# Performance work log

Measured on AMD Instinct MI355X. Metric: run time of the kernel, lower is better.

Reference implementation:

```python
import jax, jax.numpy as jnp
import numpy as np

B, T, D_MODEL = 4, 2048, 1024
D_EXPERT, N_EXPERTS, TOP_K = 4096, 8, 2
CAPACITY_FACTOR = 1.25
AUX_COEFF, Z_COEFF = 0.01, 0.001


def setup_inputs() -> dict:
    key = jax.random.key(0)
    k = jax.random.split(key, 4)
    x = jax.random.normal(k[0], (B, T, D_MODEL), jnp.float32)
    Wr = jax.random.normal(k[1], (D_MODEL, N_EXPERTS), jnp.float32) * 0.02
    W1 = jax.random.normal(k[2], (N_EXPERTS, D_MODEL, D_EXPERT), jnp.float32) * (1.0 / np.sqrt(D_MODEL))
    b1 = jnp.zeros((N_EXPERTS, D_EXPERT), jnp.float32)
    W2 = jax.random.normal(k[3], (N_EXPERTS, D_EXPERT, D_MODEL), jnp.float32) * (1.0 / np.sqrt(D_EXPERT))
    b2 = jnp.zeros((N_EXPERTS, D_MODEL), jnp.float32)
    return {"x": x, "Wr": Wr, "W1": W1, "b1": b1, "W2": W2, "b2": b2}


def reference(x, Wr, W1, b1, W2, b2):
    Bb, Tt, D = x.shape
    N = Bb * Tt
    E = W1.shape[0]
    capacity = max(1, int(N / E * CAPACITY_FACTOR * TOP_K))

    xf = x.reshape(N, D)
    logits = xf @ Wr                                    # (N, E)
    z_loss = jnp.mean(jax.nn.logsumexp(logits, axis=-1) ** 2)
    probs = jax.nn.softmax(logits, axis=-1)             # (N, E)

    topk_p, topk_i = jax.lax.top_k(probs, TOP_K)        # (N, K)
    # one-hot expert mask (top-k experts are distinct per token)
    mask = jnp.zeros((N, E), probs.dtype).at[jnp.arange(N)[:, None], topk_i].set(1.0)

    # capacity truncation: keep first `capacity` assigned tokens per expert, in token order
    pos = (jnp.cumsum(mask, axis=0) - mask).astype(jnp.int32)   # exclusive rank within expert
    keep = (pos < capacity) & (mask > 0)
    mask_t = jnp.where(keep, mask, jnp.zeros_like(mask))

    # Switch-style aux loss on truncated mask
    total_sel = jnp.maximum(mask_t.sum(), 1.0)
    f_i = mask_t.sum(axis=0) / total_sel
    P_i = probs.mean(axis=0)
    aux_loss = E * jnp.sum(f_i * P_i)

    # normalized top-k combine weights (differentiable through probs)
    tk_raw = jnp.take_along_axis(probs, topk_i, axis=1)          # (N, K)
    tk = tk_raw / jnp.maximum(tk_raw.sum(axis=-1, keepdims=True), 1e-9)

    # dispatch tokens into (E, capacity, D) buffer; dropped tokens scatter out of range
    pos_safe = jnp.where(keep, pos, capacity)                    # capacity -> dropped
    pos_k = jnp.take_along_axis(pos_safe, topk_i, axis=1)        # (N, K)
    upd = jnp.broadcast_to(xf[:, None, :], (N, TOP_K, D)).reshape(-1, D)
    buf = jnp.zeros((E, capacity, D), x.dtype).at[topk_i.reshape(-1), pos_k.reshape(-1)].set(upd, mode='drop')

    # grouped expert MLP
    h = jax.nn.relu(jnp.einsum('ecd,edf->ecf', buf, W1) + b1[:, None, :])
    eo = jnp.einsum('ecf,efd->ecd', h, W2) + b2[:, None, :]      # (E, capacity, D)

    # combine: gather each token's top-k expert outputs, weight, sum; dropped -> weight 0
    valid_k = jnp.take_along_axis(keep, topk_i, axis=1)          # (N, K) bool
    w = tk * valid_k.astype(tk.dtype)
    pos_g = jnp.minimum(pos_k, capacity - 1)
    gathered = eo[topk_i, pos_g]                                 # (N, K, D)
    out = jnp.einsum('nk,nkd->nd', w, gathered).reshape(Bb, Tt, D)

    total_aux = AUX_COEFF * aux_loss + Z_COEFF * z_loss
    return out, aux_loss, z_loss, total_aux
```

## Files before the change

kernel.cpp:

```cpp
#include <hip/hip_runtime.h>
#include <stdint.h>

#define N_TOK    8192
#define DM       1024
#define DE       4096
#define NEXP     8
#define CAP      2560
#define AUX_CO   0.01f
#define Z_CO     0.001f

typedef __attribute__((ext_vector_type(4))) float f32x4;
typedef __attribute__((ext_vector_type(8))) __bf16 bf16x8;

static __device__ __forceinline__ unsigned short f2bf(float f) {
  union { float f; uint32_t u; } v; v.f = f;
  uint32_t r = 0x7fffu + ((v.u >> 16) & 1u);
  return (unsigned short)((v.u + r) >> 16);
}
static __device__ __forceinline__ float bf2f(unsigned short u) {
  union { uint32_t u; float f; } v; v.u = ((uint32_t)u) << 16;
  return v.f;
}

#define MEMFENCE() asm volatile("" ::: "memory")
#define BAR()    do { MEMFENCE(); __builtin_amdgcn_s_barrier(); MEMFENCE(); } while (0)
#define LGKM0()  asm volatile("s_waitcnt lgkmcnt(0)" ::: "memory")
#define VMW(N)   asm volatile("s_waitcnt vmcnt(" #N ")" ::: "memory")
#define GLD16(g, l) __builtin_amdgcn_global_load_lds( \
    (const __attribute__((address_space(1))) void*)(g), \
    (__attribute__((address_space(3))) void*)(l), 16, 0, 0)

__global__ __launch_bounds__(256) void transpose_to_bf16(
    const float* __restrict__ in, unsigned short* __restrict__ out, int R, int C)
{
  __shared__ float tile[64][65];
  const size_t eoff = (size_t)blockIdx.z * R * C;
  const int bx = blockIdx.x * 64, by = blockIdx.y * 64;
  const int r = threadIdx.x >> 2, c16 = (threadIdx.x & 3) * 16;
#pragma unroll
  for (int j = 0; j < 4; ++j) {
    const float4 v = *(const float4*)&in[eoff + (size_t)(by + r) * C + bx + c16 + j * 4];
    tile[r][c16 + j * 4 + 0] = v.x; tile[r][c16 + j * 4 + 1] = v.y;
    tile[r][c16 + j * 4 + 2] = v.z; tile[r][c16 + j * 4 + 3] = v.w;
  }
  __syncthreads();
  const int oc = threadIdx.x >> 2, r16 = (threadIdx.x & 3) * 16;
#pragma unroll
  for (int half = 0; half < 2; ++half) {
    uint4 o;
    const int rb = r16 + half * 8;
    o.x = (uint32_t)f2bf(tile[rb + 0][oc]) | ((uint32_t)f2bf(tile[rb + 1][oc]) << 16);
    o.y = (uint32_t)f2bf(tile[rb + 2][oc]) | ((uint32_t)f2bf(tile[rb + 3][oc]) << 16);
    o.z = (uint32_t)f2bf(tile[rb + 4][oc]) | ((uint32_t)f2bf(tile[rb + 5][oc]) << 16);
    o.w = (uint32_t)f2bf(tile[rb + 6][oc]) | ((uint32_t)f2bf(tile[rb + 7][oc]) << 16);
    *(uint4*)&out[eoff + (size_t)(bx + oc) * R + by + rb] = o;
  }
}

__global__ __launch_bounds__(256) void router_kernel(
    const float* __restrict__ x, const float* __restrict__ Wr,
    int* __restrict__ topk, float* __restrict__ tkw, float* __restrict__ zP)
{
  const int tid = threadIdx.x, lane = tid & 63, wave = tid >> 6;
  float zacc = 0.f;
  float pacc[NEXP];
#pragma unroll
  for (int e = 0; e < NEXP; ++e) pacc[e] = 0.f;

  for (int it = 0; it < 4; ++it) {
    const int t = blockIdx.x * 16 + it * 4 + wave;
    float acc[NEXP];
#pragma unroll
    for (int e = 0; e < NEXP; ++e) acc[e] = 0.f;
    const f32x4* x4 = (const f32x4*)(x + (size_t)t * DM);
#pragma unroll
    for (int i = 0; i < 4; ++i) {
      f32x4 xv = x4[i * 64 + lane];
#pragma unroll
      for (int j = 0; j < 4; ++j) {
        const float xs = xv[j];
        const float* wr = Wr + (size_t)((i * 64 + lane) * 4 + j) * NEXP;
#pragma unroll
        for (int e = 0; e < NEXP; ++e) acc[e] += xs * wr[e];
      }
    }
#pragma unroll
    for (int m = 32; m; m >>= 1)
#pragma unroll
      for (int e = 0; e < NEXP; ++e) acc[e] += __shfl_xor(acc[e], m);

    float mx = acc[0];
#pragma unroll
    for (int e = 1; e < NEXP; ++e) mx = fmaxf(mx, acc[e]);
    float p[NEXP], s = 0.f;
#pragma unroll
    for (int e = 0; e < NEXP; ++e) { p[e] = expf(acc[e] - mx); s += p[e]; }
    const float lse = mx + logf(s);
    zacc += lse * lse;
    const float inv_s = 1.f / s;
#pragma unroll
    for (int e = 0; e < NEXP; ++e) pacc[e] += p[e] * inv_s;

    int e0 = 0; float v0 = p[0];
#pragma unroll
    for (int e = 1; e < NEXP; ++e) if (p[e] > v0) { v0 = p[e]; e0 = e; }
    int e1 = -1; float v1 = -1.f;
#pragma unroll
    for (int e = 0; e < NEXP; ++e) if (e != e0 && p[e] > v1) { v1 = p[e]; e1 = e; }

    const float pr0 = v0 * inv_s, pr1 = v1 * inv_s;
    const float denom = fmaxf(pr0 + pr1, 1e-9f);
    if (lane == 0) {
      topk[2*t]   = e0; topk[2*t+1] = e1;
      tkw[2*t]    = pr0 / denom; tkw[2*t+1] = pr1 / denom;
    }
  }
  __shared__ float blk[4][9];
  if (lane == 0) {
    blk[wave][0] = zacc;
#pragma unroll
    for (int e = 0; e < NEXP; ++e) blk[wave][1 + e] = pacc[e];
  }
  __syncthreads();
  if (tid < 9)
    zP[blockIdx.x * 9 + tid] = blk[0][tid] + blk[1][tid] + blk[2][tid] + blk[3][tid];
}

__global__ __launch_bounds__(512) void scan_kernel(
    const int2* __restrict__ topk, const float2* __restrict__ tkw,
    int* __restrict__ posk, float* __restrict__ wts,
    int* __restrict__ inv, int* __restrict__ kept)
{
  __shared__ int2   stopk[N_TOK];
  __shared__ float2 stkw[N_TOK];
  const int tid = threadIdx.x;
  for (int j = tid; j < N_TOK; j += 512) { stopk[j] = topk[j]; stkw[j] = tkw[j]; }
  __syncthreads();

  const int lane = tid & 63;
  const int e = tid >> 6;
  int base = 0;
  const uint64_t below = (lane == 63) ? 0xFFFFFFFFFFFFFFFFull >> 1
                                      : ((1ull << lane) - 1ull);
  for (int i = 0; i < N_TOK / 64; ++i) {
    const int t = i * 64 + lane;
    const int2 ti = stopk[t];
    const float2 w = stkw[t];
    const bool hit = (ti.x == e) || (ti.y == e);
    const uint64_t m = __ballot(hit);
    if (hit) {
      const int pos = base + (int)__popcll(m & below);
      const bool kp = pos < CAP;
      const int k = (ti.x == e) ? 0 : 1;
      posk[2*t + k] = kp ? pos : CAP;
      wts[2*t + k]  = kp ? ((k == 0) ? w.x : w.y) : 0.f;
      if (kp) inv[e * CAP + pos] = t;
    }
    base += (int)__popcll(m);
  }
  const int tail = base < CAP ? base : CAP;
  for (int q = tail + lane; q < CAP; q += 64) inv[e * CAP + q] = -1;
  if (lane == 0) kept[e] = tail;
}

__global__ __launch_bounds__(256) void dispatch_kernel(
    const float* __restrict__ x, const int* __restrict__ inv,
    unsigned short* __restrict__ buf)
{
  const int slot = blockIdx.x;
  const int t = inv[slot];
  ushort4 o;
  if (t >= 0) {
    const f32x4 v = ((const f32x4*)(x + (size_t)t * DM))[threadIdx.x];
    o.x = f2bf(v[0]); o.y = f2bf(v[1]); o.z = f2bf(v[2]); o.w = f2bf(v[3]);
  } else {
    o.x = 0; o.y = 0; o.z = 0; o.w = 0;
  }
  ((ushort4*)(buf + (size_t)slot * DM))[threadIdx.x] = o;
}

template<bool RELU, bool BIAS>
__global__ __launch_bounds__(512, 2) void gemm2b(
    const unsigned short* __restrict__ A,
    const unsigned short* __restrict__ Bt,
    const float* __restrict__ bias,
    unsigned short* __restrict__ C,
    const int* __restrict__ kept,
    int M, int N, int K, int lda, int mt, int nt, int nsplit, int nwg)
{
  __shared__ __attribute__((aligned(16))) unsigned short As[2 * 16384];
  __shared__ __attribute__((aligned(16))) unsigned short Bs[2 * 16384];
  const int tid = threadIdx.x, lane = tid & 63, wave = tid >> 6;
  const int wr = wave >> 2, wc = wave & 3;
  const int frow = lane & 15, kgrp = lane >> 4;

  int wg = (int)blockIdx.x;
  wg = (wg & 7) * (nwg >> 3) + (wg >> 3);
  const int ntpe = mt * nt;
  const int bpe = ntpe * nsplit;
  const int e = wg / bpe;
  const int rem = wg % bpe;
  const int split = rem / ntpe;
  const int rr = rem % ntpe;
  const int m0 = (rr / nt) * 256;
  const int n0 = (rr % nt) * 256;
  if (m0 >= kept[e]) return;

  const unsigned short* Ae = A  + (size_t)e * M * lda + (size_t)m0 * lda + (size_t)split * K;
  const unsigned short* Be = Bt + (size_t)e * N * lda + (size_t)n0 * lda + (size_t)split * K;

  const int srow = tid >> 3;
  const int scol = ((tid & 7) ^ (srow & 7)) * 8;

  auto stage = [&](int t) {
    const int c = t & 1, k0 = t * 64;
#pragma unroll
    for (int i = 0; i < 4; ++i)
      GLD16(Ae + (size_t)(i * 64 + srow) * lda + (k0 + scol),
            &As[c * 16384 + i * 4096 + tid * 8]);
#pragma unroll
    for (int i = 0; i < 4; ++i)
      GLD16(Be + (size_t)(i * 64 + srow) * lda + (k0 + scol),
            &Bs[c * 16384 + i * 4096 + tid * 8]);
  };
  auto rdA = [&](bf16x8* dst, int c, int mh) {
#pragma unroll
    for (int m = 0; m < 4; ++m) {
      const int row = wr * 128 + mh * 64 + m * 16 + frow;
#pragma unroll
      for (int kk = 0; kk < 2; ++kk)
        dst[m * 2 + kk] = *(const bf16x8*)
          &As[c * 16384 + row * 64 + (((kk * 4 + kgrp) ^ (row & 7)) * 8)];
    }
  };
  auto rdB = [&](bf16x8* dst, int c, int nh) {
#pragma unroll
    for (int n = 0; n < 2; ++n) {
      const int row = wc * 64 + nh * 32 + n * 16 + frow;
#pragma unroll
      for (int kk = 0; kk < 2; ++kk)
        dst[n * 2 + kk] = *(const bf16x8*)
          &Bs[c * 16384 + row * 64 + (((kk * 4 + kgrp) ^ (row & 7)) * 8)];
    }
  };

  f32x4 acc[8][4];
#pragma unroll
  for (int m = 0; m < 8; ++m)
#pragma unroll
    for (int n = 0; n < 4; ++n) acc[m][n] = (f32x4){0.f, 0.f, 0.f, 0.f};

  bf16x8 af0[8], af1[8], bq0[4], bq1[4];
  auto mfmaQ = [&](int mh, int nh, bf16x8* af, bf16x8* bq) {
#pragma unroll
    for (int m = 0; m < 4; ++m)
#pragma unroll
      for (int n = 0; n < 2; ++n)
#pragma unroll
        for (int kk = 0; kk < 2; ++kk)
          acc[mh * 4 + m][nh * 2 + n] = __builtin_amdgcn_mfma_f32_16x16x32_bf16(
              af[m * 2 + kk], bq[n * 2 + kk], acc[mh * 4 + m][nh * 2 + n], 0, 0, 0);
  };

  const int nk = K >> 6;

  stage(0); stage(1);

  for (int t = 0; t < nk; ++t) {
    const int c = t & 1;
    if (t + 2 <= nk) { VMW(8); } else { VMW(0); }
    BAR();
    rdA(af0, c, 0);
    rdA(af1, c, 1);
    rdB(bq0, c, 0);
    rdB(bq1, c, 1);
    LGKM0();
    BAR();
    if (t + 2 < nk) stage(t + 2);
    __builtin_amdgcn_s_setprio(1);
    mfmaQ(0, 0, af0, bq0);
    mfmaQ(0, 1, af0, bq1);
    mfmaQ(1, 0, af1, bq0);
    mfmaQ(1, 1, af1, bq1);
    __builtin_amdgcn_s_setprio(0);
  }

  unsigned short* Ce = C + (size_t)(split * NEXP + e) * M * N;
  const int r0 = m0 + wr * 128 + 4 * kgrp;
  const int c0 = n0 + wc * 64 + frow;
#pragma unroll
  for (int nf = 0; nf < 4; ++nf) {
    const int cc = c0 + nf * 16;
    float bv = 0.f;
    if (BIAS) bv = bias[(size_t)e * N + cc];
#pragma unroll
    for (int m = 0; m < 8; ++m) {
#pragma unroll
      for (int r = 0; r < 4; ++r) {
        float v = acc[m][nf][r] + bv;
        if (RELU) v = fmaxf(v, 0.f);
        Ce[(size_t)(r0 + m * 16 + r) * N + cc] = f2bf(v);
      }
    }
  }
}

__global__ __launch_bounds__(256) void combine_kernel(
    const unsigned short* __restrict__ eo2,
    const float* __restrict__ b2,
    const int* __restrict__ posk, const float* __restrict__ wts,
    const int* __restrict__ topk,
    const float* __restrict__ zP, const int* __restrict__ kept,
    float* __restrict__ out, float* __restrict__ outs)
{
  const int t = blockIdx.x;
  const int e0 = topk[2*t], e1 = topk[2*t+1];
  int p0 = posk[2*t], p1 = posk[2*t+1];
  p0 = p0 < CAP - 1 ? p0 : CAP - 1;
  p1 = p1 < CAP - 1 ? p1 : CAP - 1;
  const float w0 = wts[2*t], w1 = wts[2*t+1];
  const size_t o0 = ((size_t)e0 * CAP + p0) * DM;
  const size_t o1 = ((size_t)e1 * CAP + p1) * DM;
  const size_t sp = (size_t)NEXP * CAP * DM;
  const ushort4 a0 = ((const ushort4*)(eo2 + o0))[threadIdx.x];
  const ushort4 a1 = ((const ushort4*)(eo2 + sp + o0))[threadIdx.x];
  const ushort4 c0 = ((const ushort4*)(eo2 + o1))[threadIdx.x];
  const ushort4 c1 = ((const ushort4*)(eo2 + sp + o1))[threadIdx.x];
  const f32x4 bv0 = ((const f32x4*)(b2 + (size_t)e0 * DM))[threadIdx.x];
  const f32x4 bv1 = ((const f32x4*)(b2 + (size_t)e1 * DM))[threadIdx.x];
  f32x4 o;
  o[0] = w0 * (bf2f(a0.x) + bf2f(a1.x) + bv0[0]) + w1 * (bf2f(c0.x) + bf2f(c1.x) + bv1[0]);
  o[1] = w0 * (bf2f(a0.y) + bf2f(a1.y) + bv0[1]) + w1 * (bf2f(c0.y) + bf2f(c1.y) + bv1[1]);
  o[2] = w0 * (bf2f(a0.z) + bf2f(a1.z) + bv0[2]) + w1 * (bf2f(c0.z) + bf2f(c1.z) + bv1[2]);
  o[3] = w0 * (bf2f(a0.w) + bf2f(a1.w) + bv0[3]) + w1 * (bf2f(c0.w) + bf2f(c1.w) + bv1[3]);
  ((f32x4*)(out + (size_t)t * DM))[threadIdx.x] = o;

  if (t == 0 && threadIdx.x < 64) {
    const int lane = threadIdx.x;
    float v[9];
#pragma unroll
    for (int e = 0; e < 9; ++e) {
      float s = 0.f;
      for (int bk = 0; bk < 8; ++bk) s += zP[(lane * 8 + bk) * 9 + e];
      v[e] = s;
    }
#pragma unroll
    for (int m = 32; m; m >>= 1)
#pragma unroll
      for (int e = 0; e < 9; ++e) v[e] += __shfl_xor(v[e], m);
    if (lane == 0) {
      const float z = v[0] / (float)N_TOK;
      float total = 0.f;
      for (int e = 0; e < NEXP; ++e) total += (float)kept[e];
      total = fmaxf(total, 1.f);
      float aux = 0.f;
      for (int e = 0; e < NEXP; ++e)
        aux += ((float)kept[e] / total) * (v[1 + e] / (float)N_TOK);
      aux *= (float)NEXP;
      outs[0] = aux;
      outs[1] = z;
      outs[2] = AUX_CO * aux + Z_CO * z;
    }
  }
}

extern "C" void kernel_launch(void* const* d_in, const int* in_sizes, int n_in,
                              void* d_out, int out_size, void* d_ws, size_t ws_size,
                              hipStream_t stream)
{
  const float* x  = (const float*)d_in[0];
  const float* Wr = (const float*)d_in[1];
  const float* W1 = (const float*)d_in[2];
  const float* b1 = (const float*)d_in[3];
  const float* W2 = (const float*)d_in[4];
  const float* b2 = (const float*)d_in[5];
  float* out = (float*)d_out;

  char* p = (char*)d_ws;
  auto alloc = [&](size_t bytes) {
    char* q = p; p += (bytes + 255) & ~(size_t)255; return q;
  };
  unsigned short* W1t = (unsigned short*)alloc((size_t)NEXP * DM * DE * 2);
  unsigned short* W2t = (unsigned short*)alloc((size_t)NEXP * DM * DE * 2);
  unsigned short* buf = (unsigned short*)alloc((size_t)NEXP * CAP * DM * 2);
  unsigned short* h   = (unsigned short*)alloc((size_t)NEXP * CAP * DE * 2);
  unsigned short* eo2 = (unsigned short*)alloc((size_t)2 * NEXP * CAP * DM * 2);
  int*   topk = (int*)alloc((size_t)N_TOK * 2 * 4);
  float* tkw  = (float*)alloc((size_t)N_TOK * 2 * 4);
  int*   posk = (int*)alloc((size_t)N_TOK * 2 * 4);
  float* wts  = (float*)alloc((size_t)N_TOK * 2 * 4);
  int*   inv  = (int*)alloc((size_t)NEXP * CAP * 4);
  int*   kept = (int*)alloc((size_t)NEXP * 4);
  float* zP   = (float*)alloc((size_t)512 * 9 * 4);

  transpose_to_bf16<<<dim3(DE / 64, DM / 64, NEXP), 256, 0, stream>>>(W1, W1t, DM, DE);
  transpose_to_bf16<<<dim3(DM / 64, DE / 64, NEXP), 256, 0, stream>>>(W2, W2t, DE, DM);
  router_kernel<<<512, 256, 0, stream>>>(x, Wr, topk, tkw, zP);
  scan_kernel<<<1, 512, 0, stream>>>((const int2*)topk, (const float2*)tkw, posk, wts, inv, kept);
  dispatch_kernel<<<NEXP * CAP, 256, 0, stream>>>(x, inv, buf);

  gemm2b<true, true><<<1280, 512, 0, stream>>>(
      buf, W1t, b1, h, kept, CAP, DE, DM, DM, 10, 16, 1, 1280);
  gemm2b<false, false><<<640, 512, 0, stream>>>(
      h, W2t, nullptr, eo2, kept, CAP, DM, DE / 2, DE, 10, 4, 2, 640);

  combine_kernel<<<N_TOK, 256, 0, stream>>>(eo2, b2, posk, wts, topk, zP, kept,
                                            out, out + (size_t)N_TOK * DM);
}
```

Measured before the change: 556.3 us.

## Shrink expert GEMM tiles to 128x256 with K=32 steps for higher occupancy

The grouped expert GEMM tile shrinks from 256x256 with K-step 64 to 128x256 with K-step 32, and the LDS swizzle and fragment loads are reworked to match. This cuts LDS use and accumulator registers so four workgroups can fit per CU, and doubles the grid size. The finer M granularity also skips more tiles beyond each expert's kept count. In exchange, arithmetic intensity per tile drops, barriers per FLOP double, and global traffic for B rises.

```diff
diff --git a/kernel.cpp b/kernel.cpp
--- a/kernel.cpp
+++ b/kernel.cpp
@@ -180,7 +180,7 @@
 }
 
 template<bool RELU, bool BIAS>
-__global__ __launch_bounds__(512, 2) void gemm2b(
+__global__ __launch_bounds__(512, 4) void gemmT(
     const unsigned short* __restrict__ A,
     const unsigned short* __restrict__ Bt,
     const float* __restrict__ bias,
@@ -188,8 +188,8 @@
     const int* __restrict__ kept,
     int M, int N, int K, int lda, int mt, int nt, int nsplit, int nwg)
 {
-  __shared__ __attribute__((aligned(16))) unsigned short As[2 * 16384];
-  __shared__ __attribute__((aligned(16))) unsigned short Bs[2 * 16384];
+  __shared__ __attribute__((aligned(16))) unsigned short As[2 * 4096];
+  __shared__ __attribute__((aligned(16))) unsigned short Bs[2 * 8192];
   const int tid = threadIdx.x, lane = tid & 63, wave = tid >> 6;
   const int wr = wave >> 2, wc = wave & 3;
   const int frow = lane & 15, kgrp = lane >> 4;
@@ -202,91 +202,75 @@
   const int rem = wg % bpe;
   const int split = rem / ntpe;
   const int rr = rem % ntpe;
-  const int m0 = (rr / nt) * 256;
+  const int m0 = (rr / nt) * 128;
   const int n0 = (rr % nt) * 256;
   if (m0 >= kept[e]) return;
 
   const unsigned short* Ae = A  + (size_t)e * M * lda + (size_t)m0 * lda + (size_t)split * K;
   const unsigned short* Be = Bt + (size_t)e * N * lda + (size_t)n0 * lda + (size_t)split * K;
 
-  const int srow = tid >> 3;
-  const int scol = ((tid & 7) ^ (srow & 7)) * 8;
+  const int srow = tid >> 2;
+  const int sg   = tid & 3;
 
   auto stage = [&](int t) {
-    const int c = t & 1, k0 = t * 64;
-#pragma unroll
-    for (int i = 0; i < 4; ++i)
-      GLD16(Ae + (size_t)(i * 64 + srow) * lda + (k0 + scol),
-            &As[c * 16384 + i * 4096 + tid * 8]);
-#pragma unroll
-    for (int i = 0; i < 4; ++i)
-      GLD16(Be + (size_t)(i * 64 + srow) * lda + (k0 + scol),
-            &Bs[c * 16384 + i * 4096 + tid * 8]);
+    const int c = t & 1, k0 = t * 32;
+    {
+      const int gcol = sg ^ ((srow >> 1) & 3);
+      GLD16(Ae + (size_t)srow * lda + (k0 + gcol * 8), &As[c * 4096 + tid * 8]);
+    }
+#pragma unroll
+    for (int i = 0; i < 2; ++i) {
+      const int row = i * 128 + srow;
+      const int gcol = sg ^ ((row >> 1) & 3);
+      GLD16(Be + (size_t)row * lda + (k0 + gcol * 8), &Bs[c * 8192 + i * 4096 + tid * 8]);
+    }
   };
-  auto rdA = [&](bf16x8* dst, int c, int mh) {
+  auto rdA = [&](bf16x8* dst, int c) {
 #pragma unroll
     for (int m = 0; m < 4; ++m) {
-      const int row = wr * 128 + mh * 64 + m * 16 + frow;
-#pragma unroll
-      for (int kk = 0; kk < 2; ++kk)
-        dst[m * 2 + kk] = *(const bf16x8*)
-          &As[c * 16384 + row * 64 + (((kk * 4 + kgrp) ^ (row & 7)) * 8)];
+      const int row = wr * 64 + m * 16 + frow;
+      dst[m] = *(const bf16x8*)&As[c * 4096 + row * 32 + ((kgrp ^ ((row >> 1) & 3)) * 8)];
     }
   };
-  auto rdB = [&](bf16x8* dst, int c, int nh) {
-#pragma unroll
-    for (int n = 0; n < 2; ++n) {
-      const int row = wc * 64 + nh * 32 + n * 16 + frow;
-#pragma unroll
-      for (int kk = 0; kk < 2; ++kk)
-        dst[n * 2 + kk] = *(const bf16x8*)
-          &Bs[c * 16384 + row * 64 + (((kk * 4 + kgrp) ^ (row & 7)) * 8)];
+  auto rdB = [&](bf16x8* dst, int c) {
+#pragma unroll
+    for (int n = 0; n < 4; ++n) {
+      const int row = wc * 64 + n * 16 + frow;
+      dst[n] = *(const bf16x8*)&Bs[c * 8192 + row * 32 + ((kgrp ^ ((row >> 1) & 3)) * 8)];
     }
   };
 
-  f32x4 acc[8][4];
-#pragma unroll
-  for (int m = 0; m < 8; ++m)
+  f32x4 acc[4][4];
+#pragma unroll
+  for (int m = 0; m < 4; ++m)
 #pragma unroll
     for (int n = 0; n < 4; ++n) acc[m][n] = (f32x4){0.f, 0.f, 0.f, 0.f};
-
-  bf16x8 af0[8], af1[8], bq0[4], bq1[4];
-  auto mfmaQ = [&](int mh, int nh, bf16x8* af, bf16x8* bq) {
-#pragma unroll
-    for (int m = 0; m < 4; ++m)
-#pragma unroll
-      for (int n = 0; n < 2; ++n)
-#pragma unroll
-        for (int kk = 0; kk < 2; ++kk)
-          acc[mh * 4 + m][nh * 2 + n] = __builtin_amdgcn_mfma_f32_16x16x32_bf16(
-              af[m * 2 + kk], bq[n * 2 + kk], acc[mh * 4 + m][nh * 2 + n], 0, 0, 0);
-  };
-
-  const int nk = K >> 6;
+  bf16x8 af[4], bq[4];
+
+  const int nk = K >> 5;
 
   stage(0); stage(1);
 
   for (int t = 0; t < nk; ++t) {
     const int c = t & 1;
-    if (t + 2 <= nk) { VMW(8); } else { VMW(0); }
+    if (t + 2 <= nk) { VMW(3); } else { VMW(0); }
     BAR();
-    rdA(af0, c, 0);
-    rdA(af1, c, 1);
-    rdB(bq0, c, 0);
-    rdB(bq1, c, 1);
+    rdA(af, c);
+    rdB(bq, c);
     LGKM0();
     BAR();
     if (t + 2 < nk) stage(t + 2);
     __builtin_amdgcn_s_setprio(1);
-    mfmaQ(0, 0, af0, bq0);
-    mfmaQ(0, 1, af0, bq1);
-    mfmaQ(1, 0, af1, bq0);
-    mfmaQ(1, 1, af1, bq1);
+#pragma unroll
+    for (int m = 0; m < 4; ++m)
+#pragma unroll
+      for (int n = 0; n < 4; ++n)
+        acc[m][n] = __builtin_amdgcn_mfma_f32_16x16x32_bf16(af[m], bq[n], acc[m][n], 0, 0, 0);
     __builtin_amdgcn_s_setprio(0);
   }
 
   unsigned short* Ce = C + (size_t)(split * NEXP + e) * M * N;
-  const int r0 = m0 + wr * 128 + 4 * kgrp;
+  const int r0 = m0 + wr * 64 + 4 * kgrp;
   const int c0 = n0 + wc * 64 + frow;
 #pragma unroll
   for (int nf = 0; nf < 4; ++nf) {
@@ -294,7 +278,7 @@
     float bv = 0.f;
     if (BIAS) bv = bias[(size_t)e * N + cc];
 #pragma unroll
-    for (int m = 0; m < 8; ++m) {
+    for (int m = 0; m < 4; ++m) {
 #pragma unroll
       for (int r = 0; r < 4; ++r) {
         float v = acc[m][nf][r] + bv;
@@ -399,10 +383,10 @@
   scan_kernel<<<1, 512, 0, stream>>>((const int2*)topk, (const float2*)tkw, posk, wts, inv, kept);
   dispatch_kernel<<<NEXP * CAP, 256, 0, stream>>>(x, inv, buf);
 
-  gemm2b<true, true><<<1280, 512, 0, stream>>>(
-      buf, W1t, b1, h, kept, CAP, DE, DM, DM, 10, 16, 1, 1280);
-  gemm2b<false, false><<<640, 512, 0, stream>>>(
-      h, W2t, nullptr, eo2, kept, CAP, DM, DE / 2, DE, 10, 4, 2, 640);
+  gemmT<true, true><<<2560, 512, 0, stream>>>(
+      buf, W1t, b1, h, kept, CAP, DE, DM, DM, 20, 16, 1, 2560);
+  gemmT<false, false><<<1280, 512, 0, stream>>>(
+      h, W2t, nullptr, eo2, kept, CAP, DM, DE / 2, DE, 20, 4, 2, 1280);
 
   combine_kernel<<<N_TOK, 256, 0, stream>>>(eo2, b2, posk, wts, topk, zP, kept,
                                             out, out + (size_t)N_TOK * DM);
```

After: 529.2 us. 4.9% less time.
